# Optimization experiments

Hardware: AMD Instinct MI355X
Metric: run time of the kernel (lower is better)

## Reference

```python
import jax, jax.numpy as jnp
import numpy as np

SCALING = 128.0 / 64  # alpha / rank = 2.0
EPS = 1e-8


def setup_inputs() -> dict:
    key = jax.random.key(0)
    ks = jax.random.split(key, 5)
    B, S, D_IN, D_OUT, R = 2, 4096, 4096, 4096, 64
    x = jax.random.normal(ks[0], (B, S, D_IN), dtype=jnp.float32)
    base_output = jax.random.normal(ks[1], (B, S, D_OUT), dtype=jnp.float32)
    base_weight = jax.random.normal(ks[2], (D_OUT, D_IN), dtype=jnp.float32) * 0.02
    lora_A = jax.random.normal(ks[3], (R, D_IN), dtype=jnp.float32) * 0.02
    lora_B = jax.random.normal(ks[4], (D_OUT, R), dtype=jnp.float32) * 0.02
    magnitude = jnp.ones((D_OUT,), dtype=jnp.float32)
    return {"x": x, "base_output": base_output, "base_weight": base_weight,
            "lora_A": lora_A, "lora_B": lora_B, "magnitude": magnitude}


def reference(x, base_output, base_weight, lora_A, lora_B, magnitude):
    # LoRA path: x @ A^T @ B^T, scaled  (dropout p=0 -> identity)
    xa = jnp.einsum('bsd,rd->bsr', x, lora_A)          # [B,S,r]
    delta_v = jnp.einsum('bsr,or->bso', xa, lora_B) * SCALING  # [B,S,out]
    # Updated weight and its per-row L2 norm
    updated_weight = base_weight + (lora_B @ lora_A) * SCALING  # [out,in]
    updated_norm = jnp.sqrt(jnp.sum(updated_weight * updated_weight, axis=1))  # [out]
    mag_scale = magnitude / (updated_norm + EPS)  # [out]
    combined = base_output + delta_v
    return combined * mag_scale[None, None, :]
```

## Files before the change

kernel.cpp:

```cpp
#include <hip/hip_runtime.h>
#include <math.h>

typedef __bf16 bf16x8 __attribute__((ext_vector_type(8)));
typedef float f32x4 __attribute__((ext_vector_type(4)));

#define MFMA16(a, b, c) __builtin_amdgcn_mfma_f32_16x16x32_bf16(a, b, c, 0, 0, 0)

static constexpr int M_TOT = 8192;
static constexpr int DIN = 4096;
static constexpr int DOUT = 4096;
static constexpr int RNK = 64;

__device__ inline unsigned short f2bf(float f) {
    union { float f; unsigned u; } v; v.f = f;
    unsigned r = v.u + 0x7FFFu + ((v.u >> 16) & 1u);
    return (unsigned short)(r >> 16);
}

__device__ inline void gload_lds16(const float* g, char* lds_base) {
    __builtin_amdgcn_global_load_lds(
        (const __attribute__((address_space(1))) void*)g,
        (__attribute__((address_space(3))) void*)lds_base, 16, 0, 0);
}

__global__ __launch_bounds__(256) void k_prep(const float* __restrict__ A,
                                              const float* __restrict__ B,
                                              unsigned short* __restrict__ Afrag,
                                              unsigned short* __restrict__ Atfrag,
                                              unsigned short* __restrict__ Bfrag) {
    int i = blockIdx.x * 256 + threadIdx.x;
    unsigned short ab = f2bf(A[i]);
    int n = i >> 12, k = i & 4095;
    Afrag[(((k >> 5) << 2) + (n >> 4)) * 512 +
          ((((k >> 3) & 3) << 4) + (n & 15)) * 8 + (k & 7)] = ab;
    Atfrag[(((k >> 4) << 1) + (n >> 5)) * 512 +
           ((((n >> 3) & 3) << 4) + (k & 15)) * 8 + (n & 7)] = ab;
    unsigned short bb = f2bf(B[i]);
    int o = i >> 6, r = i & 63;
    Bfrag[(((o >> 4) << 1) + (r >> 5)) * 512 +
          ((((r >> 3) & 3) << 4) + (o & 15)) * 8 + (r & 7)] = bb;
}

__global__ __launch_bounds__(256) void kAB(const float* __restrict__ x,
                                           const unsigned short* __restrict__ Afrag,
                                           float* __restrict__ pxa,
                                           const float* __restrict__ bw,
                                           const unsigned short* __restrict__ Bfrag,
                                           const unsigned short* __restrict__ Atfrag,
                                           float* __restrict__ pn) {
    __shared__ __align__(16) char smem[33024];
    char* buf0 = smem;
    char* buf1 = smem + 16384;
    int tid = threadIdx.x;
    int wid = tid >> 6, lane = tid & 63;
    int row = lane & 15, kq = lane >> 4;
    int lane8 = lane * 8;
    int swzr = (row & 7) << 4;
    int sub = blockIdx.x >> 1;

    if ((blockIdx.x & 1) == 0) {
        float (*red)[1024] = (float (*)[1024])smem;
        int mt = sub & 511, kpart = sub >> 9;
        int m0 = mt * 16;
        const float* xbase = x + (size_t)m0 * DIN + kpart * 2048;

        f32x4 acc0 = {0.f, 0.f, 0.f, 0.f};
        f32x4 acc1 = acc0, acc2 = acc0, acc3 = acc0;
        bf16x8 setA[8], setB[8];

        auto STAGE = [&](char* buf, int c) {
            #pragma unroll
            for (int j = 0; j < 4; ++j) {
                int r = wid * 4 + j;
                int srcb = (lane * 16) ^ ((r & 7) << 4);
                const float* g = xbase + (size_t)r * DIN + c * 256 + (srcb >> 2);
                gload_lds16(g, buf + r * 1024);
            }
        };
        auto AFRAG = [&](bf16x8* set, int c) {
            #pragma unroll
            for (int s = 0; s < 2; ++s) {
                int ks = kpart * 64 + c * 8 + wid * 2 + s;
                const unsigned short* ap = Afrag + (size_t)ks * 2048 + lane8;
                set[s * 4 + 0] = *(const bf16x8*)(ap);
                set[s * 4 + 1] = *(const bf16x8*)(ap + 512);
                set[s * 4 + 2] = *(const bf16x8*)(ap + 1024);
                set[s * 4 + 3] = *(const bf16x8*)(ap + 1536);
            }
        };
        auto COMPUTE = [&](const char* buf, const bf16x8* set) {
            #pragma unroll
            for (int s = 0; s < 2; ++s) {
                int kbyte = wid * 256 + s * 128 + kq * 32;
                f32x4 xlo = *(const f32x4*)(buf + row * 1024 + ((kbyte) ^ swzr));
                f32x4 xhi = *(const f32x4*)(buf + row * 1024 + ((kbyte + 16) ^ swzr));
                bf16x8 af;
                #pragma unroll
                for (int j = 0; j < 4; ++j) {
                    af[j] = (__bf16)xlo[j];
                    af[j + 4] = (__bf16)xhi[j];
                }
                acc0 = MFMA16(af, set[s * 4 + 0], acc0);
                acc1 = MFMA16(af, set[s * 4 + 1], acc1);
                acc2 = MFMA16(af, set[s * 4 + 2], acc2);
                acc3 = MFMA16(af, set[s * 4 + 3], acc3);
            }
        };

        STAGE(buf0, 0); AFRAG(setA, 0);
        __syncthreads();
        #pragma unroll
        for (int c = 0; c < 8; c += 2) {
            if (c + 1 < 8) { STAGE(buf1, c + 1); AFRAG(setB, c + 1); }
            COMPUTE(buf0, setA);
            __syncthreads();
            if (c + 2 < 8) { STAGE(buf0, c + 2); AFRAG(setA, c + 2); }
            if (c + 1 < 8) COMPUTE(buf1, setB);
            __syncthreads();
        }

        int mb = kq * 4;
        #pragma unroll
        for (int rg = 0; rg < 4; ++rg) {
            red[wid][(mb + rg) * 64 + row]      = acc0[rg];
            red[wid][(mb + rg) * 64 + 16 + row] = acc1[rg];
            red[wid][(mb + rg) * 64 + 32 + row] = acc2[rg];
            red[wid][(mb + rg) * 64 + 48 + row] = acc3[rg];
        }
        __syncthreads();
        #pragma unroll
        for (int e = tid; e < 1024; e += 256) {
            float s = red[0][e] + red[1][e] + red[2][e] + red[3][e];
            pxa[(size_t)kpart * M_TOT * RNK + (size_t)(m0 + (e >> 6)) * RNK + (e & 63)] = s;
        }
    } else {
        float (*part)[16] = (float (*)[16])(smem + 32768);
        int ot = sub & 255, ipart = sub >> 8;
        int o0 = ot * 16;
        const float* bwbase = bw + (size_t)o0 * DIN + ipart * 1024;

        bf16x8 b0 = *(const bf16x8*)(Bfrag + (size_t)(ot * 2) * 512 + lane8);
        bf16x8 b1 = *(const bf16x8*)(Bfrag + (size_t)(ot * 2 + 1) * 512 + lane8);

        f32x4 nacc = {0.f, 0.f, 0.f, 0.f};
        bf16x8 setA[8], setB[8];

        auto STAGE = [&](char* buf, int c) {
            #pragma unroll
            for (int j = 0; j < 4; ++j) {
                int r = wid * 4 + j;
                int srcb = (lane * 16) ^ ((r & 7) << 4);
                const float* g = bwbase + (size_t)r * DIN + c * 256 + (srcb >> 2);
                gload_lds16(g, buf + r * 1024);
            }
        };
        auto ATFRAG = [&](bf16x8* set, int c) {
            #pragma unroll
            for (int g = 0; g < 4; ++g) {
                int it = ipart * 64 + c * 16 + wid * 4 + g;
                const unsigned short* atp = Atfrag + (size_t)it * 1024 + lane8;
                set[g * 2]     = *(const bf16x8*)(atp);
                set[g * 2 + 1] = *(const bf16x8*)(atp + 512);
            }
        };
        auto COMPUTE = [&](const char* buf, const bf16x8* set) {
            #pragma unroll
            for (int g = 0; g < 4; ++g) {
                f32x4 d = {0.f, 0.f, 0.f, 0.f};
                d = MFMA16(set[g * 2], b0, d);
                d = MFMA16(set[g * 2 + 1], b1, d);
                int ibyte = wid * 256 + g * 64 + kq * 16;
                f32x4 wv = *(const f32x4*)(buf + row * 1024 + (ibyte ^ swzr));
                #pragma unroll
                for (int rg = 0; rg < 4; ++rg) {
                    float w = wv[rg] + 2.0f * d[rg];
                    nacc[rg] += w * w;
                }
            }
        };

        STAGE(buf0, 0); ATFRAG(setA, 0);
        __syncthreads();
        #pragma unroll
        for (int c = 0; c < 4; c += 2) {
            if (c + 1 < 4) { STAGE(buf1, c + 1); ATFRAG(setB, c + 1); }
            COMPUTE(buf0, setA);
            __syncthreads();
            if (c + 2 < 4) { STAGE(buf0, c + 2); ATFRAG(setA, c + 2); }
            if (c + 1 < 4) COMPUTE(buf1, setB);
            __syncthreads();
        }

        float ns = nacc[0] + nacc[1] + nacc[2] + nacc[3];
        ns += __shfl_xor(ns, 16, 64);
        ns += __shfl_xor(ns, 32, 64);
        if (kq == 0) part[wid][row] = ns;
        __syncthreads();
        if (tid < 16)
            pn[ipart * DOUT + o0 + tid] =
                part[0][tid] + part[1][tid] + part[2][tid] + part[3][tid];
    }
}

__global__ __launch_bounds__(256) void kfin(const float* __restrict__ pxa,
                                            unsigned short* __restrict__ xafrag,
                                            const float* __restrict__ pn,
                                            const float* __restrict__ mag,
                                            float* __restrict__ mscale) {
    int tid = threadIdx.x;
    if (blockIdx.x < 512) {
        int mt = blockIdx.x;
        int e0 = tid * 4;
        size_t o = (size_t)(mt * 16 + (e0 >> 6)) * RNK + (e0 & 63);
        f32x4 s0 = *(const f32x4*)(pxa + o);
        f32x4 s1 = *(const f32x4*)(pxa + (size_t)M_TOT * RNK + o);
        int ml = e0 >> 6, r0 = e0 & 63;
        ushort4 h;
        h.x = f2bf(s0[0] + s1[0]);
        h.y = f2bf(s0[1] + s1[1]);
        h.z = f2bf(s0[2] + s1[2]);
        h.w = f2bf(s0[3] + s1[3]);
        *(ushort4*)&xafrag[((size_t)(mt * 2 + (r0 >> 5))) * 512 +
                           ((((r0 >> 3) & 3) << 4) + ml) * 8 + (r0 & 7)] = h;
    } else {
        int o = (int)(blockIdx.x - 512) * 256 + tid;
        float n2 = pn[o] + pn[DOUT + o] + pn[2 * DOUT + o] + pn[3 * DOUT + o];
        mscale[o] = mag[o] / (sqrtf(n2) + 1e-8f);
    }
}

__global__ __launch_bounds__(256) void kB(const float* __restrict__ base,
                                          const unsigned short* __restrict__ xafrag,
                                          const unsigned short* __restrict__ Bfrag,
                                          const float* __restrict__ mscale,
                                          float* __restrict__ out) {
    __shared__ float dls[32][260];
    int tid = threadIdx.x;
    int wid = tid >> 6, lane = tid & 63;
    int row = lane & 15, kq = lane >> 4;
    int m0 = blockIdx.x * 32;
    int n0 = blockIdx.y * 256;
    int col = n0 + lane * 4;
    int lane8 = lane * 8;

    f32x4 bpre[2][4];
    #pragma unroll
    for (int h = 0; h < 2; ++h)
        #pragma unroll
        for (int r = 0; r < 4; ++r)
            bpre[h][r] = __builtin_nontemporal_load(
                (const f32x4*)(base + (size_t)(m0 + h * 16 + wid * 4 + r) * DOUT + col));
    f32x4 msv = *(const f32x4*)(mscale + col);

    bf16x8 xb0[2], xb1[2];
    #pragma unroll
    for (int h = 0; h < 2; ++h) {
        size_t mt = (size_t)(blockIdx.x * 2 + h);
        xb0[h] = *(const bf16x8*)(xafrag + (mt * 2) * 512 + lane8);
        xb1[h] = *(const bf16x8*)(xafrag + (mt * 2 + 1) * 512 + lane8);
    }

    #pragma unroll
    for (int nt = 0; nt < 4; ++nt) {
        size_t ntg = (size_t)((n0 + wid * 64 + nt * 16) >> 4);
        bf16x8 a0 = *(const bf16x8*)(Bfrag + (ntg * 2) * 512 + lane8);
        bf16x8 a1 = *(const bf16x8*)(Bfrag + (ntg * 2 + 1) * 512 + lane8);
        #pragma unroll
        for (int h = 0; h < 2; ++h) {
            f32x4 acc = {0.f, 0.f, 0.f, 0.f};
            acc = MFMA16(a0, xb0[h], acc);
            acc = MFMA16(a1, xb1[h], acc);
            *(f32x4*)&dls[h * 16 + row][wid * 64 + nt * 16 + kq * 4] = acc;
        }
    }
    __syncthreads();

    #pragma unroll
    for (int h = 0; h < 2; ++h)
        #pragma unroll
        for (int r = 0; r < 4; ++r) {
            int m = h * 16 + wid * 4 + r;
            f32x4 d = *(const f32x4*)&dls[m][lane * 4];
            size_t gidx = (size_t)(m0 + m) * DOUT + col;
            f32x4 o;
            #pragma unroll
            for (int j = 0; j < 4; ++j) o[j] = (bpre[h][r][j] + 2.0f * d[j]) * msv[j];
            __builtin_nontemporal_store(o, (f32x4*)(out + gidx));
        }
}

extern "C" void kernel_launch(void* const* d_in, const int* in_sizes, int n_in,
                              void* d_out, int out_size, void* d_ws, size_t ws_size,
                              hipStream_t stream) {
    const float* x    = (const float*)d_in[0];
    const float* base = (const float*)d_in[1];
    const float* bw   = (const float*)d_in[2];
    const float* lA   = (const float*)d_in[3];
    const float* lB   = (const float*)d_in[4];
    const float* mag  = (const float*)d_in[5];
    float* out = (float*)d_out;

    char* ws = (char*)d_ws;
    unsigned short* Afrag  = (unsigned short*)(ws);
    unsigned short* Atfrag = (unsigned short*)(ws + (512u << 10));
    unsigned short* Bfrag  = (unsigned short*)(ws + (1024u << 10));
    unsigned short* xafrag = (unsigned short*)(ws + (1536u << 10));
    float*          pxa    = (float*)(ws + (2560u << 10));
    float*          pn     = (float*)(ws + (6656u << 10));
    float*          msc    = (float*)(ws + (6720u << 10));

    hipLaunchKernelGGL(k_prep, dim3(1024), dim3(256), 0, stream, lA, lB, Afrag, Atfrag, Bfrag);
    hipLaunchKernelGGL(kAB, dim3(2048), dim3(256), 0, stream,
                       x, Afrag, pxa, bw, Bfrag, Atfrag, pn);
    hipLaunchKernelGGL(kfin, dim3(528), dim3(256), 0, stream, pxa, xafrag, pn, mag, msc);
    hipLaunchKernelGGL(kB, dim3(M_TOT / 32, DOUT / 256), dim3(256), 0, stream,
                       base, xafrag, Bfrag, msc, out);
}
```

Measured before the change: 108.1 us.

## Keep two stages of loads in flight using partial vmcnt waits

```diff
diff --git a/kernel.cpp b/kernel.cpp
--- a/kernel.cpp
+++ b/kernel.cpp
@@ -5,6 +5,11 @@
 typedef float f32x4 __attribute__((ext_vector_type(4)));
 
 #define MFMA16(a, b, c) __builtin_amdgcn_mfma_f32_16x16x32_bf16(a, b, c, 0, 0, 0)
+
+#define VMCNT12() asm volatile("s_waitcnt vmcnt(12)" ::: "memory")
+#define VMCNT0()  asm volatile("s_waitcnt vmcnt(0)" ::: "memory")
+#define SFENCE()  __builtin_amdgcn_sched_barrier(0)
+#define BAR()     __builtin_amdgcn_s_barrier()
 
 static constexpr int M_TOT = 8192;
 static constexpr int DIN = 4096;
@@ -107,17 +112,24 @@
             }
         };
 
-        STAGE(buf0, 0); AFRAG(setA, 0);
-        __syncthreads();
-        #pragma unroll
-        for (int c = 0; c < 8; c += 2) {
-            if (c + 1 < 8) { STAGE(buf1, c + 1); AFRAG(setB, c + 1); }
+        STAGE(buf0, 0); AFRAG(setA, 0); SFENCE();
+        STAGE(buf1, 1); AFRAG(setB, 1); SFENCE();
+        #pragma unroll
+        for (int c = 0; c < 6; c += 2) {
+            VMCNT12(); BAR(); SFENCE();
             COMPUTE(buf0, setA);
-            __syncthreads();
-            if (c + 2 < 8) { STAGE(buf0, c + 2); AFRAG(setA, c + 2); }
-            if (c + 1 < 8) COMPUTE(buf1, setB);
-            __syncthreads();
-        }
+            SFENCE(); BAR();
+            STAGE(buf0, c + 2); AFRAG(setA, c + 2); SFENCE();
+            VMCNT12(); BAR(); SFENCE();
+            COMPUTE(buf1, setB);
+            SFENCE(); BAR();
+            STAGE(buf1, c + 3); AFRAG(setB, c + 3); SFENCE();
+        }
+        VMCNT12(); BAR(); SFENCE();
+        COMPUTE(buf0, setA);
+        SFENCE(); BAR();
+        VMCNT0(); BAR(); SFENCE();
+        COMPUTE(buf1, setB);
 
         int mb = kq * 4;
         #pragma unroll
@@ -179,17 +191,21 @@
             }
         };
 
-        STAGE(buf0, 0); ATFRAG(setA, 0);
-        __syncthreads();
-        #pragma unroll
-        for (int c = 0; c < 4; c += 2) {
-            if (c + 1 < 4) { STAGE(buf1, c + 1); ATFRAG(setB, c + 1); }
-            COMPUTE(buf0, setA);
-            __syncthreads();
-            if (c + 2 < 4) { STAGE(buf0, c + 2); ATFRAG(setA, c + 2); }
-            if (c + 1 < 4) COMPUTE(buf1, setB);
-            __syncthreads();
-        }
+        STAGE(buf0, 0); ATFRAG(setA, 0); SFENCE();
+        STAGE(buf1, 1); ATFRAG(setB, 1); SFENCE();
+        VMCNT12(); BAR(); SFENCE();
+        COMPUTE(buf0, setA);
+        SFENCE(); BAR();
+        STAGE(buf0, 2); ATFRAG(setA, 2); SFENCE();
+        VMCNT12(); BAR(); SFENCE();
+        COMPUTE(buf1, setB);
+        SFENCE(); BAR();
+        STAGE(buf1, 3); ATFRAG(setB, 3); SFENCE();
+        VMCNT12(); BAR(); SFENCE();
+        COMPUTE(buf0, setA);
+        SFENCE(); BAR();
+        VMCNT0(); BAR(); SFENCE();
+        COMPUTE(buf1, setB);
 
         float ns = nacc[0] + nacc[1] + nacc[2] + nacc[3];
         ns += __shfl_xor(ns, 16, 64);
```

Measured after the change: 108.6 us, median of 2. Within noise of the previous version (+0.5%).
